# Performance work log

Measured on AMD Instinct MI355X. Metric: run time of the kernel, lower is better.

The kernel has to match this reference:

```python
import jax, jax.numpy as jnp
import numpy as np

NUM_HEADS = 16


def setup_inputs() -> dict:
    key = jax.random.key(0)
    ks = jax.random.split(key, 5)
    B, L, D = 2, 2048, 1024
    x = jax.random.normal(ks[0], (B, L, D), dtype=jnp.float32)
    s = 1.0 / np.sqrt(D)
    Wqkv_w = jax.random.normal(ks[1], (3 * D, D), dtype=jnp.float32) * s
    Wqkv_b = jax.random.normal(ks[2], (3 * D,), dtype=jnp.float32) * 0.01
    out_w = jax.random.normal(ks[3], (D, D), dtype=jnp.float32) * s
    out_b = jax.random.normal(ks[4], (D,), dtype=jnp.float32) * 0.01
    return {"x": x, "Wqkv_w": Wqkv_w, "Wqkv_b": Wqkv_b, "out_w": out_w, "out_b": out_b}


def reference(x, Wqkv_w, Wqkv_b, out_w, out_b):
    B, L, D = x.shape
    H = NUM_HEADS
    d = D // H
    scale = 1.0 / np.sqrt(d).astype(np.float32)
    # qkv projection: torch Linear is x @ W^T + b
    qkv = x @ Wqkv_w.T + Wqkv_b                      # [B, L, 3D]
    qkv = qkv.reshape(B, L, 3, H, d)                 # (three h d) split
    qkv = jnp.transpose(qkv, (2, 0, 3, 1, 4))        # [3, B, H, L, d]
    q, k, v = qkv[0], qkv[1], qkv[2]
    k = k * scale
    # Linear-attention recurrence S_t = S_{t-1} + v_t k_t^T, y_t = S_t q_t
    # == causally-masked unnormalized attention: y_t = sum_{s<=t} (q_t.k_s) v_s
    scores = jnp.einsum('bhld,bhmd->bhlm', q, k)     # [B,H,L,L]
    causal = jnp.tril(jnp.ones((L, L), dtype=scores.dtype))
    y = jnp.einsum('bhlm,bhmd->bhld', scores * causal, v)  # [B,H,L,d]
    y = jnp.transpose(y, (0, 2, 1, 3)).reshape(B, L, D)    # b l (h d)
    return y @ out_w.T + out_b
```

## Files before the change

kernel.cpp:

```cpp
#include <hip/hip_runtime.h>


#define DEV __device__ __forceinline__

typedef __attribute__((ext_vector_type(8))) short bf16x8;
typedef __attribute__((ext_vector_type(4))) float f32x4;

DEV ushort f2bf(float f) {
  union { float f; unsigned u; } v; v.f = f;
  unsigned r = v.u + 0x7fffu + ((v.u >> 16) & 1u);
  return (ushort)(r >> 16);
}
DEV float bf2f(unsigned b) {
  union { unsigned u; float f; } v; v.u = (b & 0xffffu) << 16;
  return v.f;
}
DEV void glds16(const ushort* g, ushort* l) {
  __builtin_amdgcn_global_load_lds(
      (const __attribute__((address_space(1))) unsigned int*)g,
      (__attribute__((address_space(3))) unsigned int*)l, 16, 0, 0);
}

__global__ __launch_bounds__(256) void cvt_all(const float* __restrict__ x,
                                               const float* __restrict__ Ww,
                                               const float* __restrict__ Ow,
                                               ushort* __restrict__ xb,
                                               ushort* __restrict__ wqkvb,
                                               ushort* __restrict__ outwb) {
  int i = blockIdx.x * 256 + threadIdx.x;
  const float* src; ushort* dst; int off;
  if (i < 1048576)      { src = x;  dst = xb;    off = i; }
  else if (i < 1835008) { src = Ww; dst = wqkvb; off = i - 1048576; }
  else                  { src = Ow; dst = outwb; off = i - 1835008; }
  float4 v = ((const float4*)src)[off];
  ushort4 o;
  o.x = f2bf(v.x); o.y = f2bf(v.y); o.z = f2bf(v.z); o.w = f2bf(v.w);
  ((ushort4*)dst)[off] = o;
}

template <bool OUT_BF16, bool KSCALE>
__global__ __launch_bounds__(256) void gemm_bt(const ushort* __restrict__ A,
                                               const ushort* __restrict__ Bw,
                                               const float* __restrict__ bias,
                                               void* __restrict__ Cout,
                                               int M, int N, int K) {
  __shared__ ushort As[128 * 32];
  __shared__ ushort Bs[128 * 32];
  const int t = threadIdx.x;
  const int wid = t >> 6, lane = t & 63;
  const int quad = lane >> 4, l16 = lane & 15;
  const int g = blockIdx.x;
  const int j = g >> 3;
  const int bx = (g & 7) * 3 + j % 3;
  const int by = j / 3;
  const int bm = by * 128, bn = bx * 128;
  const int wm = (wid >> 1) * 64, wn = (wid & 1) * 64;

  f32x4 acc[4][4];
  const f32x4 z = {0.f, 0.f, 0.f, 0.f};
#pragma unroll
  for (int i = 0; i < 4; ++i)
#pragma unroll
    for (int jj = 0; jj < 4; ++jj) acc[i][jj] = z;

  const ushort* ag = A + (size_t)(bm + (t >> 2)) * K + ((t & 3) * 8);
  const ushort* bg = Bw + (size_t)(bn + (t >> 2)) * K + ((t & 3) * 8);
  ushort* asl = As + wid * 512;
  ushort* bsl = Bs + wid * 512;
  const size_t rowskip = (size_t)64 * K;

  for (int k0 = 0; k0 < K; k0 += 32) {
    glds16(ag + k0, asl);
    glds16(ag + k0 + rowskip, asl + 2048);
    glds16(bg + k0, bsl);
    glds16(bg + k0 + rowskip, bsl + 2048);
    __syncthreads();
    bf16x8 af[4], bf[4];
#pragma unroll
    for (int i = 0; i < 4; ++i) {
      af[i] = *(const bf16x8*)(As + (wm + i * 16 + l16) * 32 + quad * 8);
      bf[i] = *(const bf16x8*)(Bs + (wn + i * 16 + l16) * 32 + quad * 8);
    }
#pragma unroll
    for (int i = 0; i < 4; ++i)
#pragma unroll
      for (int jj = 0; jj < 4; ++jj)
        acc[i][jj] = __builtin_amdgcn_mfma_f32_16x16x32_bf16(af[i], bf[jj], acc[i][jj], 0, 0, 0);
    __syncthreads();
  }

#pragma unroll
  for (int i = 0; i < 4; ++i)
#pragma unroll
    for (int jj = 0; jj < 4; ++jj) {
      const int col = bn + wn + jj * 16 + l16;
      const float bv = bias[col];
      float sc = 1.f;
      if (KSCALE) sc = ((col >> 10) == 1) ? 0.125f : 1.f;
#pragma unroll
      for (int r = 0; r < 4; ++r) {
        const int row = bm + wm + i * 16 + quad * 4 + r;
        const float v = (acc[i][jj][r] + bv) * sc;
        if (OUT_BF16)
          ((ushort*)Cout)[(size_t)row * N + col] = f2bf(v);
        else
          ((float*)Cout)[(size_t)row * N + col] = v;
      }
    }
}

__global__ __launch_bounds__(256) void gemm_out64(const ushort* __restrict__ A,
                                                  const ushort* __restrict__ Bw,
                                                  const float* __restrict__ bias,
                                                  float* __restrict__ C,
                                                  int M, int N, int K) {
  __shared__ ushort As[64 * 32];
  __shared__ ushort Bs[128 * 32];
  const int t = threadIdx.x;
  const int wid = t >> 6, lane = t & 63;
  const int quad = lane >> 4, l16 = lane & 15;
  const int g = blockIdx.x;
  const int bm = (g >> 3) * 64, bn = (g & 7) * 128;
  const int wn = wid * 32;

  f32x4 acc[4][2];
  const f32x4 z = {0.f, 0.f, 0.f, 0.f};
#pragma unroll
  for (int i = 0; i < 4; ++i) { acc[i][0] = z; acc[i][1] = z; }

  const ushort* ag = A + (size_t)(bm + (t >> 2)) * K + ((t & 3) * 8);
  const ushort* bg = Bw + (size_t)(bn + (t >> 2)) * K + ((t & 3) * 8);
  ushort* asl = As + wid * 512;
  ushort* bsl = Bs + wid * 512;
  const size_t rowskip = (size_t)64 * K;

  for (int k0 = 0; k0 < K; k0 += 32) {
    glds16(ag + k0, asl);
    glds16(bg + k0, bsl);
    glds16(bg + k0 + rowskip, bsl + 2048);
    __syncthreads();
    bf16x8 af[4], bf[2];
#pragma unroll
    for (int i = 0; i < 4; ++i)
      af[i] = *(const bf16x8*)(As + (i * 16 + l16) * 32 + quad * 8);
#pragma unroll
    for (int jj = 0; jj < 2; ++jj)
      bf[jj] = *(const bf16x8*)(Bs + (wn + jj * 16 + l16) * 32 + quad * 8);
#pragma unroll
    for (int i = 0; i < 4; ++i)
#pragma unroll
      for (int jj = 0; jj < 2; ++jj)
        acc[i][jj] = __builtin_amdgcn_mfma_f32_16x16x32_bf16(af[i], bf[jj], acc[i][jj], 0, 0, 0);
    __syncthreads();
  }

#pragma unroll
  for (int i = 0; i < 4; ++i)
#pragma unroll
    for (int jj = 0; jj < 2; ++jj) {
      const int col = bn + wn + jj * 16 + l16;
      const float bv = bias[col];
#pragma unroll
      for (int r = 0; r < 4; ++r) {
        const int row = bm + i * 16 + quad * 4 + r;
        C[(size_t)row * N + col] = acc[i][jj][r] + bv;
      }
    }
}

__global__ __launch_bounds__(256) void kv_local(const ushort* __restrict__ qkv,
                                                float* __restrict__ mlocT,
                                                ushort* __restrict__ vTg) {
  const int c = blockIdx.x, bh = blockIdx.y;
  const int b = bh >> 4, hd = bh & 15;
  const int t = threadIdx.x;
  const int wid = t >> 6, lane = t & 63;
  const int quad = lane >> 4, l16 = lane & 15;
  __shared__ ushort kT[64 * 136];
  __shared__ ushort vT[64 * 136];

  {
    const int row = t & 127;
    const int isv = t >> 7;
    const ushort* gp = qkv + (size_t)(b * 2048 + c * 128 + row) * 3072 +
                       1024 + isv * 1024 + hd * 64;
    ushort tmp[64];
#pragma unroll
    for (int q = 0; q < 8; ++q) *(uint4*)(tmp + q * 8) = *(const uint4*)(gp + q * 8);
    ushort* dst = isv ? vT : kT;
#pragma unroll
    for (int j = 0; j < 64; ++j) dst[j * 136 + row] = tmp[j];
  }
  __syncthreads();

  {
    const int row = t >> 2, seg = t & 3;
    const ushort* src = vT + row * 136 + seg * 32;
    ushort* dst = vTg + ((size_t)bh * 16 + c) * 8192 + row * 128 + seg * 32;
#pragma unroll
    for (int q = 0; q < 4; ++q)
      *(uint4*)(dst + q * 8) = *(const uint4*)(src + q * 8);
  }

  const f32x4 z = {0.f, 0.f, 0.f, 0.f};
  f32x4 acc[4];
#pragma unroll
  for (int ct = 0; ct < 4; ++ct) acc[ct] = z;
#pragma unroll
  for (int kc = 0; kc < 4; ++kc) {
    bf16x8 afr = *(const bf16x8*)(vT + (wid * 16 + l16) * 136 + kc * 32 + quad * 8);
#pragma unroll
    for (int ct = 0; ct < 4; ++ct) {
      bf16x8 bfr = *(const bf16x8*)(kT + (ct * 16 + l16) * 136 + kc * 32 + quad * 8);
      acc[ct] = __builtin_amdgcn_mfma_f32_16x16x32_bf16(afr, bfr, acc[ct], 0, 0, 0);
    }
  }

  float* outp = mlocT + ((size_t)bh * 16 + c) * 4096;
#pragma unroll
  for (int ct = 0; ct < 4; ++ct)
#pragma unroll
    for (int r = 0; r < 4; ++r)
      outp[(wid * 16 + quad * 4 + r) * 64 + ct * 16 + l16] = acc[ct][r];
}

__global__ __launch_bounds__(256) void kv_prefix(const float* __restrict__ mlocT,
                                                 ushort* __restrict__ statesT) {
  const int slice = blockIdx.x, bh = blockIdx.y;
  const int eidx = slice * 256 + threadIdx.x;
  float run = 0.f;
  for (int c = 0; c < 16; ++c) {
    const size_t idx = ((size_t)bh * 16 + c) * 4096 + eidx;
    statesT[idx] = f2bf(run);
    run += mlocT[idx];
  }
}

__global__ __launch_bounds__(256) void attn_chunk(const ushort* __restrict__ qkv,
                                                  const ushort* __restrict__ statesT,
                                                  const ushort* __restrict__ vTg,
                                                  ushort* __restrict__ yb) {
  const int c = blockIdx.x, bh = blockIdx.y;
  const int b = bh >> 4, hd = bh & 15;
  const int l0 = c * 128;
  const int t = threadIdx.x;
  const int wid = t >> 6, lane = t & 63;
  const int quad = lane >> 4, l16 = lane & 15;

  __shared__ ushort P[16384];
  __shared__ ushort U[16384];
  ushort* Qs = U;
  ushort* Ks = U + 8192;
  ushort* vT = U;
  ushort* sT = U + 8704;

  {
    uint4 zz; zz.x = zz.y = zz.z = zz.w = 0u;
    uint4* p4 = (uint4*)P;
#pragma unroll
    for (int i = 0; i < 8; ++i) p4[i * 256 + t] = zz;
  }
  {
    const int kcs = ((lane & 7) ^ (lane >> 3)) * 8;
    const ushort* qg = qkv + (size_t)(b * 2048 + l0 + (t >> 3)) * 3072 + hd * 64 + kcs;
    ushort* ql = Qs + wid * 512;
    ushort* kl = Ks + wid * 512;
#pragma unroll
    for (int h2 = 0; h2 < 4; ++h2) {
      glds16(qg + (size_t)h2 * 32 * 3072, ql + h2 * 2048);
      glds16(qg + (size_t)h2 * 32 * 3072 + 1024, kl + h2 * 2048);
    }
  }
  __syncthreads();

  bf16x8 qf[2][2];
#pragma unroll
  for (int i = 0; i < 2; ++i) {
    const int rt = (i == 0) ? wid : 7 - wid;
#pragma unroll
    for (int kc = 0; kc < 2; ++kc)
      qf[i][kc] = *(const bf16x8*)(Qs + (rt * 16 + l16) * 64 +
                                   (((kc * 4 + quad) ^ (l16 & 7)) * 8));
  }

  const f32x4 z4 = {0.f, 0.f, 0.f, 0.f};
  f32x4 pacc[2][8];
#pragma unroll
  for (int i = 0; i < 2; ++i)
#pragma unroll
    for (int jj = 0; jj < 8; ++jj) pacc[i][jj] = z4;

#pragma unroll
  for (int i = 0; i < 2; ++i) {
    const int rt = (i == 0) ? wid : 7 - wid;
#pragma unroll
    for (int tj = 0; tj < 8; ++tj) {
      if (tj <= rt) {
#pragma unroll
        for (int kc = 0; kc < 2; ++kc) {
          bf16x8 kfr = *(const bf16x8*)(Ks + (tj * 16 + l16) * 64 +
                                        (((kc * 4 + quad) ^ (l16 & 7)) * 8));
          pacc[i][tj] = __builtin_amdgcn_mfma_f32_16x16x32_bf16(qf[i][kc], kfr, pacc[i][tj], 0, 0, 0);
        }
      }
    }
  }
  __syncthreads();

  {
    const ushort* vgb = vTg + ((size_t)bh * 16 + c) * 8192;
#pragma unroll
    for (int h = 0; h < 4; ++h) {
      const int gch = (wid * 4 + h) * 64 + lane;
      const int e = gch >> 4;
      const int sc = (gch & 15) ^ (e & 7);
      glds16(vgb + e * 128 + sc * 8, vT + (wid * 4 + h) * 512);
    }
  }
#pragma unroll
  for (int i = 0; i < 2; ++i) {
    const int rt = (i == 0) ? wid : 7 - wid;
#pragma unroll
    for (int tj = 0; tj < 8; ++tj) {
      if (tj <= rt) {
#pragma unroll
        for (int r = 0; r < 4; ++r) {
          const int row = rt * 16 + quad * 4 + r;
          const int scol = tj * 16 + l16;
          const float v = (scol <= row) ? pacc[i][tj][r] : 0.f;
          P[row * 128 + (((scol >> 3) ^ (row & 7)) * 8) + (scol & 7)] = f2bf(v);
        }
      }
    }
  }
  {
    const ushort* sg = statesT + ((size_t)bh * 16 + c) * 4096;
#pragma unroll
    for (int h = 0; h < 2; ++h) {
      const int cc = h * 256 + t;
      uint4 d = *(const uint4*)(sg + cc * 8);
      *(uint4*)(sT + (cc >> 3) * 72 + (cc & 7) * 8) = d;
    }
  }
  __syncthreads();

  f32x4 yacc[2][4];
#pragma unroll
  for (int i = 0; i < 2; ++i)
#pragma unroll
    for (int jj = 0; jj < 4; ++jj) yacc[i][jj] = z4;

#pragma unroll
  for (int i = 0; i < 2; ++i) {
    const int rt = (i == 0) ? wid : 7 - wid;
    const int kcmax = rt >> 1;
#pragma unroll
    for (int kc = 0; kc < 4; ++kc) {
      if (kc <= kcmax) {
        const int prow = rt * 16 + l16;
        bf16x8 pf;
        *(uint4*)&pf = *(const uint4*)(P + prow * 128 + (((kc * 4 + quad) ^ (prow & 7)) * 8));
#pragma unroll
        for (int ct = 0; ct < 4; ++ct) {
          const int e = ct * 16 + l16;
          bf16x8 vf = *(const bf16x8*)(vT + e * 128 + (((kc * 4 + quad) ^ (e & 7)) * 8));
          yacc[i][ct] = __builtin_amdgcn_mfma_f32_16x16x32_bf16(pf, vf, yacc[i][ct], 0, 0, 0);
        }
      }
    }
#pragma unroll
    for (int kc = 0; kc < 2; ++kc) {
#pragma unroll
      for (int ct = 0; ct < 4; ++ct) {
        bf16x8 sf = *(const bf16x8*)(sT + (ct * 16 + l16) * 72 + kc * 32 + quad * 8);
        yacc[i][ct] = __builtin_amdgcn_mfma_f32_16x16x32_bf16(qf[i][kc], sf, yacc[i][ct], 0, 0, 0);
      }
    }
  }
  __syncthreads();

#pragma unroll
  for (int i = 0; i < 2; ++i) {
    const int rt = (i == 0) ? wid : 7 - wid;
#pragma unroll
    for (int ct = 0; ct < 4; ++ct)
#pragma unroll
      for (int r = 0; r < 4; ++r)
        P[(rt * 16 + quad * 4 + r) * 72 + ct * 16 + l16] = f2bf(yacc[i][ct][r]);
  }
  __syncthreads();

  {
    const int row = t >> 1, seg = t & 1;
    const ushort* src = P + row * 72 + seg * 32;
    ushort* dst = yb + (size_t)(b * 2048 + l0 + row) * 1024 + hd * 64 + seg * 32;
#pragma unroll
    for (int q = 0; q < 4; ++q)
      *(uint4*)(dst + q * 8) = *(const uint4*)(src + q * 8);
  }
}

extern "C" void kernel_launch(void* const* d_in, const int* in_sizes, int n_in,
                              void* d_out, int out_size, void* d_ws, size_t ws_size,
                              hipStream_t stream) {
  const float* x  = (const float*)d_in[0];
  const float* Ww = (const float*)d_in[1];
  const float* Wb = (const float*)d_in[2];
  const float* Ow = (const float*)d_in[3];
  const float* Ob = (const float*)d_in[4];
  float* out = (float*)d_out;

  char* ws = (char*)d_ws;
  ushort* xb      = (ushort*)(ws);
  ushort* vTg     = (ushort*)(ws);
  ushort* wqkvb   = (ushort*)(ws + (size_t)8  * 1024 * 1024);
  ushort* outwb   = (ushort*)(ws + (size_t)14 * 1024 * 1024);
  ushort* qkvb    = (ushort*)(ws + (size_t)16 * 1024 * 1024);
  float*  mlocT   = (float*) (ws + (size_t)40 * 1024 * 1024);
  ushort* statesT = (ushort*)(ws + (size_t)48 * 1024 * 1024);
  ushort* yb      = (ushort*)(ws + (size_t)52 * 1024 * 1024);

  cvt_all<<<8192, 256, 0, stream>>>(x, Ww, Ow, xb, wqkvb, outwb);
  gemm_bt<true, true><<<768, 256, 0, stream>>>(xb, wqkvb, Wb, (void*)qkvb, 4096, 3072, 1024);
  kv_local<<<dim3(16, 32), 256, 0, stream>>>(qkvb, mlocT, vTg);
  kv_prefix<<<dim3(16, 32), 256, 0, stream>>>(mlocT, statesT);
  attn_chunk<<<dim3(16, 32), 256, 0, stream>>>(qkvb, statesT, vTg, yb);
  gemm_out64<<<512, 256, 0, stream>>>(yb, outwb, Ob, out, 4096, 1024, 1024);
}
```

Baseline: 168.8 us.

## Shrink attention LDS via per-wave P slabs, read states from global, fewer barriers

Replaces the shared 128x128 P tile with a per-wave 16-row slab. P is written and consumed one row-tile at a time, so LDS drops from 64KB to 48KB and the zero-fill pass is removed. The state matrix is now read directly from global memory as MFMA operands instead of being staged in LDS, and the V load is issued earlier to overlap with the QK MFMAs. Output is written per wave through the slab, which removes two block barriers. Launch bounds request 3 blocks per CU, which raises occupancy but may cause register spills, and the uncoalesced global state reads add latency.

Result: no change. 168.5 us (-0.2%).

```diff
diff --git a/kernel.cpp b/kernel.cpp
--- a/kernel.cpp
+++ b/kernel.cpp
@@ -236,10 +236,10 @@
   }
 }
 
-__global__ __launch_bounds__(256) void attn_chunk(const ushort* __restrict__ qkv,
-                                                  const ushort* __restrict__ statesT,
-                                                  const ushort* __restrict__ vTg,
-                                                  ushort* __restrict__ yb) {
+__global__ __launch_bounds__(256, 3) void attn_chunk(const ushort* __restrict__ qkv,
+                                                     const ushort* __restrict__ statesT,
+                                                     const ushort* __restrict__ vTg,
+                                                     ushort* __restrict__ yb) {
   const int c = blockIdx.x, bh = blockIdx.y;
   const int b = bh >> 4, hd = bh & 15;
   const int l0 = c * 128;
@@ -247,19 +247,13 @@
   const int wid = t >> 6, lane = t & 63;
   const int quad = lane >> 4, l16 = lane & 15;
 
-  __shared__ ushort P[16384];
   __shared__ ushort U[16384];
+  __shared__ ushort Pb[8192];
   ushort* Qs = U;
   ushort* Ks = U + 8192;
   ushort* vT = U;
-  ushort* sT = U + 8704;
-
-  {
-    uint4 zz; zz.x = zz.y = zz.z = zz.w = 0u;
-    uint4* p4 = (uint4*)P;
-#pragma unroll
-    for (int i = 0; i < 8; ++i) p4[i * 256 + t] = zz;
-  }
+  ushort* slab = Pb + wid * 2048;
+
   {
     const int kcs = ((lane & 7) ^ (lane >> 3)) * 8;
     const ushort* qg = qkv + (size_t)(b * 2048 + l0 + (t >> 3)) * 3072 + hd * 64 + kcs;
@@ -282,6 +276,18 @@
       qf[i][kc] = *(const bf16x8*)(Qs + (rt * 16 + l16) * 64 +
                                    (((kc * 4 + quad) ^ (l16 & 7)) * 8));
   }
+  __syncthreads();
+
+  {
+    const ushort* vgb = vTg + ((size_t)bh * 16 + c) * 8192;
+#pragma unroll
+    for (int h = 0; h < 4; ++h) {
+      const int gch = (wid * 4 + h) * 64 + lane;
+      const int e = gch >> 4;
+      const int sc = (gch & 15) ^ (e & 7);
+      glds16(vgb + e * 128 + sc * 8, vT + (wid * 4 + h) * 512);
+    }
+  }
 
   const f32x4 z4 = {0.f, 0.f, 0.f, 0.f};
   f32x4 pacc[2][8];
@@ -305,61 +311,56 @@
       }
     }
   }
+
+  {
+    const int rt = wid;
+    const int tjmax = rt | 1;
+#pragma unroll
+    for (int tj = 0; tj < 8; ++tj) {
+      if (tj <= tjmax) {
+#pragma unroll
+        for (int r = 0; r < 4; ++r) {
+          const int rl = quad * 4 + r;
+          const int scol = tj * 16 + l16;
+          const float v = (scol <= rt * 16 + rl && tj <= rt) ? pacc[0][tj][r] : 0.f;
+          slab[rl * 128 + (((scol >> 3) ^ (rl & 7)) * 8) + (scol & 7)] = f2bf(v);
+        }
+      }
+    }
+  }
   __syncthreads();
 
-  {
-    const ushort* vgb = vTg + ((size_t)bh * 16 + c) * 8192;
-#pragma unroll
-    for (int h = 0; h < 4; ++h) {
-      const int gch = (wid * 4 + h) * 64 + lane;
-      const int e = gch >> 4;
-      const int sc = (gch & 15) ^ (e & 7);
-      glds16(vgb + e * 128 + sc * 8, vT + (wid * 4 + h) * 512);
-    }
-  }
+  const ushort* sg = statesT + ((size_t)bh * 16 + c) * 4096;
+  f32x4 yacc[2][4];
+#pragma unroll
+  for (int i = 0; i < 2; ++i)
+#pragma unroll
+    for (int jj = 0; jj < 4; ++jj) yacc[i][jj] = z4;
+
 #pragma unroll
   for (int i = 0; i < 2; ++i) {
     const int rt = (i == 0) ? wid : 7 - wid;
-#pragma unroll
-    for (int tj = 0; tj < 8; ++tj) {
-      if (tj <= rt) {
-#pragma unroll
-        for (int r = 0; r < 4; ++r) {
-          const int row = rt * 16 + quad * 4 + r;
-          const int scol = tj * 16 + l16;
-          const float v = (scol <= row) ? pacc[i][tj][r] : 0.f;
-          P[row * 128 + (((scol >> 3) ^ (row & 7)) * 8) + (scol & 7)] = f2bf(v);
+    if (i == 1) {
+      const int tjmax = rt | 1;
+#pragma unroll
+      for (int tj = 0; tj < 8; ++tj) {
+        if (tj <= tjmax) {
+#pragma unroll
+          for (int r = 0; r < 4; ++r) {
+            const int rl = quad * 4 + r;
+            const int scol = tj * 16 + l16;
+            const float v = (scol <= rt * 16 + rl && tj <= rt) ? pacc[1][tj][r] : 0.f;
+            slab[rl * 128 + (((scol >> 3) ^ (rl & 7)) * 8) + (scol & 7)] = f2bf(v);
+          }
         }
       }
     }
-  }
-  {
-    const ushort* sg = statesT + ((size_t)bh * 16 + c) * 4096;
-#pragma unroll
-    for (int h = 0; h < 2; ++h) {
-      const int cc = h * 256 + t;
-      uint4 d = *(const uint4*)(sg + cc * 8);
-      *(uint4*)(sT + (cc >> 3) * 72 + (cc & 7) * 8) = d;
-    }
-  }
-  __syncthreads();
-
-  f32x4 yacc[2][4];
-#pragma unroll
-  for (int i = 0; i < 2; ++i)
-#pragma unroll
-    for (int jj = 0; jj < 4; ++jj) yacc[i][jj] = z4;
-
-#pragma unroll
-  for (int i = 0; i < 2; ++i) {
-    const int rt = (i == 0) ? wid : 7 - wid;
     const int kcmax = rt >> 1;
 #pragma unroll
     for (int kc = 0; kc < 4; ++kc) {
       if (kc <= kcmax) {
-        const int prow = rt * 16 + l16;
         bf16x8 pf;
-        *(uint4*)&pf = *(const uint4*)(P + prow * 128 + (((kc * 4 + quad) ^ (prow & 7)) * 8));
+        *(uint4*)&pf = *(const uint4*)(slab + l16 * 128 + (((kc * 4 + quad) ^ (l16 & 7)) * 8));
 #pragma unroll
         for (int ct = 0; ct < 4; ++ct) {
           const int e = ct * 16 + l16;
@@ -372,12 +373,11 @@
     for (int kc = 0; kc < 2; ++kc) {
 #pragma unroll
       for (int ct = 0; ct < 4; ++ct) {
-        bf16x8 sf = *(const bf16x8*)(sT + (ct * 16 + l16) * 72 + kc * 32 + quad * 8);
+        bf16x8 sf = *(const bf16x8*)(sg + (ct * 16 + l16) * 64 + kc * 32 + quad * 8);
         yacc[i][ct] = __builtin_amdgcn_mfma_f32_16x16x32_bf16(qf[i][kc], sf, yacc[i][ct], 0, 0, 0);
       }
     }
   }
-  __syncthreads();
 
 #pragma unroll
   for (int i = 0; i < 2; ++i) {
@@ -386,17 +386,12 @@
     for (int ct = 0; ct < 4; ++ct)
 #pragma unroll
       for (int r = 0; r < 4; ++r)
-        P[(rt * 16 + quad * 4 + r) * 72 + ct * 16 + l16] = f2bf(yacc[i][ct][r]);
-  }
-  __syncthreads();
-
-  {
-    const int row = t >> 1, seg = t & 1;
-    const ushort* src = P + row * 72 + seg * 32;
-    ushort* dst = yb + (size_t)(b * 2048 + l0 + row) * 1024 + hd * 64 + seg * 32;
-#pragma unroll
-    for (int q = 0; q < 4; ++q)
-      *(uint4*)(dst + q * 8) = *(const uint4*)(src + q * 8);
+        slab[(quad * 4 + r) * 72 + ct * 16 + l16] = f2bf(yacc[i][ct][r]);
+    const int rl = lane >> 2, seg = lane & 3;
+    const ushort* src = slab + rl * 72 + seg * 16;
+    ushort* dst = yb + (size_t)(b * 2048 + l0 + rt * 16 + rl) * 1024 + hd * 64 + seg * 16;
+    *(uint4*)(dst + 0) = *(const uint4*)(src + 0);
+    *(uint4*)(dst + 8) = *(const uint4*)(src + 8);
   }
 }
 
```
